# Performance work log

Hardware: AMD Instinct MI355X
Metric: run time of the kernel (lower is better)

The kernel has to match this reference:

```python
import jax, jax.numpy as jnp
import numpy as np
from jax.ops import segment_sum, segment_max

N_NODES = 50000
N_GRAPHS = 64
EPS = 1e-16


def gat_layer(x, src, dst, W, a_src, a_dst, b, n_nodes):
    # PyG GATConv, heads=1: shared linear, additive attention, per-dst softmax
    h = x @ W                                  # [N, H]
    al_s = h @ a_src                           # [N]
    al_d = h @ a_dst                           # [N]
    e = jax.nn.leaky_relu(al_s[src] + al_d[dst], 0.2)   # [E]
    # numerically stable segment softmax over edges grouped by dst
    m = segment_max(e, dst, num_segments=n_nodes)
    m = jnp.where(jnp.isfinite(m), m, 0.0)
    ex = jnp.exp(e - m[dst])
    denom = segment_sum(ex, dst, num_segments=n_nodes)
    alpha = ex / (denom[dst] + EPS)            # [E]
    out = segment_sum(alpha[:, None] * h[src], dst, num_segments=n_nodes)
    return out + b


def setup_inputs() -> dict:
    key = jax.random.key(0)
    ks = jax.random.split(key, 16)
    H = 128
    x = jax.random.normal(ks[0], (N_NODES, 4), dtype=jnp.float32)
    edge_index = jax.random.randint(ks[1], (2, 800000), 0, N_NODES, dtype=jnp.int64)
    batch = jnp.sort(jax.random.randint(ks[2], (N_NODES,), 0, N_GRAPHS, dtype=jnp.int64))

    def glorot(k, shape):
        lim = np.sqrt(6.0 / (shape[0] + shape[-1]))
        return jax.random.uniform(k, shape, jnp.float32, -lim, lim)

    params = {
        'W1': glorot(ks[3], (4, H)), 'as1': glorot(ks[4], (H,)), 'ad1': glorot(ks[5], (H,)), 'b1': jnp.zeros((H,), jnp.float32),
        'W2': glorot(ks[6], (H, H)), 'as2': glorot(ks[7], (H,)), 'ad2': glorot(ks[8], (H,)), 'b2': jnp.zeros((H,), jnp.float32),
        'W3': glorot(ks[9], (H, H)), 'as3': glorot(ks[10], (H,)), 'ad3': glorot(ks[11], (H,)), 'b3': jnp.zeros((H,), jnp.float32),
        'Wlin': glorot(ks[12], (H, 2)), 'blin': jnp.zeros((2,), jnp.float32),
    }
    return {'x': x, 'edge_index': edge_index, 'batch': batch, **params}


def reference(x, edge_index, batch, W1, as1, ad1, b1, W2, as2, ad2, b2, W3, as3, ad3, b3, Wlin, blin):
    n = x.shape[0]
    # GATConv default add_self_loops=True
    loop = jnp.arange(n, dtype=edge_index.dtype)
    src = jnp.concatenate([edge_index[0], loop])
    dst = jnp.concatenate([edge_index[1], loop])

    h = jax.nn.relu(gat_layer(x, src, dst, W1, as1, ad1, b1, n))
    h = jax.nn.relu(gat_layer(h, src, dst, W2, as2, ad2, b2, n))
    h = gat_layer(h, src, dst, W3, as3, ad3, b3, n)

    # global_mean_pool
    sums = segment_sum(h, batch, num_segments=N_GRAPHS)          # [G, H]
    cnt = segment_sum(jnp.ones((n,), h.dtype), batch, num_segments=N_GRAPHS)
    pooled = sums / jnp.maximum(cnt, 1.0)[:, None]
    # dropout p=0.5 is identity in eval mode
    return pooled @ Wlin + blin                                   # [G, 2]
```

## Files before the change

kernel.cpp:

```cpp
#include <hip/hip_runtime.h>
#include <math.h>


#define BW 512
#define PART_CHUNK 4096
#define HIST_WGS 64

typedef __attribute__((ext_vector_type(8))) short short8v;
typedef __attribute__((ext_vector_type(4))) float f32x4;
typedef __attribute__((ext_vector_type(4))) unsigned uint4v;
typedef __attribute__((ext_vector_type(2))) unsigned uint2v;

__device__ int g_hist_ctr;

__device__ __forceinline__ float bflo(unsigned u) { return __uint_as_float(u << 16); }
__device__ __forceinline__ float bfhi(unsigned u) { return __uint_as_float(u & 0xffff0000u); }
__device__ __forceinline__ unsigned pk2bf(float a, float b) {
  unsigned ua = __float_as_uint(a); ua += 0x7fffu + ((ua >> 16) & 1u);
  unsigned ub = __float_as_uint(b); ub += 0x7fffu + ((ub >> 16) & 1u);
  return (ua >> 16) | (ub & 0xffff0000u);
}

__global__ __launch_bounds__(256) void kb_hist(const int* __restrict__ ei,
                                               int* __restrict__ bpart,
                                               int* __restrict__ bbase,
                                               int* __restrict__ bcur,
                                               int* __restrict__ rowp,
                                               int E, int ET, int N, int NB) {
  __shared__ int h[128];
  __shared__ int isLast;
  int tid = threadIdx.x;
  if (tid < 128) h[tid] = 0;
  __syncthreads();
  int stride = HIST_WGS * 256;
  for (int i = blockIdx.x * 256 + tid; i < ET; i += stride) {
    int dst = (i < E) ? ei[E + i] : (i - E);
    atomicAdd(&h[dst >> 9], 1);
  }
  __syncthreads();
  if (tid < 128) bpart[blockIdx.x * 128 + tid] = h[tid];
  __threadfence();
  if (tid == 0) {
    int old = atomicAdd(&g_hist_ctr, 1);
    isLast = (((old + 1) % HIST_WGS) == 0) ? 1 : 0;
  }
  __syncthreads();
  if (isLast) {
    __shared__ int sm[128];
    int v = 0;
    if (tid < 128) {
      for (int w = 0; w < HIST_WGS; ++w)
        v += atomicAdd(&bpart[w * 128 + tid], 0);
      if (tid >= NB) v = 0;
      sm[tid] = v;
    }
    __syncthreads();
    for (int off = 1; off < 128; off <<= 1) {
      int u = (tid < 128 && tid >= off) ? sm[tid - off] : 0;
      __syncthreads();
      if (tid < 128) sm[tid] += u;
      __syncthreads();
    }
    if (tid < 128) {
      int pre = sm[tid] - v;
      if (tid <= NB) bbase[tid] = pre;
      if (tid < NB) bcur[tid] = pre;
      if (tid == 0) rowp[N] = ET;
    }
  }
}

__global__ __launch_bounds__(256) void kb_part(const int* __restrict__ ei,
                                               int* __restrict__ bcur,
                                               int* __restrict__ bucketed,
                                               int E, int ET, int NB) {
  __shared__ int hist[128];
  __shared__ int runb[128];
  int tid = threadIdx.x;
  int base = blockIdx.x * PART_CHUNK;
  if (tid < 128) hist[tid] = 0;

  int sv[16], dv[16];
#pragma unroll
  for (int k = 0; k < 16; ++k) {
    int j = base + k * 256 + tid;
    int s = -1, d = 0;
    if (j < ET) {
      if (j < E) { s = ei[j]; d = ei[E + j]; }
      else       { s = j - E; d = j - E; }
    }
    sv[k] = s; dv[k] = d;
  }
  __syncthreads();
#pragma unroll
  for (int k = 0; k < 16; ++k)
    if (sv[k] >= 0) atomicAdd(&hist[dv[k] >> 9], 1);
  __syncthreads();
  if (tid < NB && hist[tid] > 0) runb[tid] = atomicAdd(&bcur[tid], hist[tid]);
  __syncthreads();
  if (tid < 128) hist[tid] = 0;
  __syncthreads();
#pragma unroll
  for (int k = 0; k < 16; ++k) {
    if (sv[k] >= 0) {
      int b = dv[k] >> 9;
      int off = atomicAdd(&hist[b], 1);
      bucketed[runb[b] + off] = (sv[k] << 9) | (dv[k] & (BW - 1));
    }
  }
}

__global__ __launch_bounds__(256) void kb_csrprep(const int* __restrict__ bucketed,
                                                  const int* __restrict__ bbase,
                                                  int* __restrict__ rowp,
                                                  int* __restrict__ csr,
                                                  const float* __restrict__ W2,
                                                  const float* __restrict__ W3,
                                                  const float* __restrict__ W1,
                                                  const float* __restrict__ as1,
                                                  const float* __restrict__ ad1,
                                                  unsigned short* __restrict__ Wcm2,
                                                  unsigned short* __restrict__ Wcm3,
                                                  float* __restrict__ wv,
                                                  float* __restrict__ gsum,
                                                  int N, int NB) {
  int tid = threadIdx.x;
  if ((int)blockIdx.x >= NB) {
    int pb = blockIdx.x - NB;
    if (pb >= 65) {
      int idx = (pb - 65) * 256 + tid;
      if (idx < 64 * 128 + 64) gsum[idx] = 0.f;
      return;
    }
    if (pb == 64) {
      if (tid >= 64) return;
      float2 a = *(const float2*)(as1 + tid * 2);
      float2 d = *(const float2*)(ad1 + tid * 2);
      float ps[4], pd[4];
#pragma unroll
      for (int k = 0; k < 4; ++k) {
        float2 w = *(const float2*)(W1 + k * 128 + tid * 2);
        ps[k] = w.x * a.x + w.y * a.y;
        pd[k] = w.x * d.x + w.y * d.y;
      }
      for (int off = 32; off; off >>= 1) {
#pragma unroll
        for (int k = 0; k < 4; ++k) {
          ps[k] += __shfl_xor(ps[k], off);
          pd[k] += __shfl_xor(pd[k], off);
        }
      }
      if (tid == 0) {
#pragma unroll
        for (int k = 0; k < 4; ++k) { wv[k] = ps[k]; wv[4 + k] = pd[k]; }
      }
      return;
    }
    int i = pb * 256 + tid;
    if (i < 16384) {
      int k = i >> 7, n = i & 127;
      unsigned u = __float_as_uint(W2[i]); u += 0x7fffu + ((u >> 16) & 1u);
      Wcm2[n * 128 + k] = (unsigned short)(u >> 16);
      unsigned v = __float_as_uint(W3[i]); v += 0x7fffu + ((v >> 16) & 1u);
      Wcm3[n * 128 + k] = (unsigned short)(v >> 16);
    }
    return;
  }
  __shared__ int h[512];
  __shared__ int sm[256];
  __shared__ int cur[512];
  int b = blockIdx.x;
  int cb = bbase[b], ce = bbase[b + 1];

  h[tid] = 0; h[tid + 256] = 0;
  __syncthreads();
  for (int j = cb + tid; j < ce; j += 256)
    atomicAdd(&h[bucketed[j] & (BW - 1)], 1);
  __syncthreads();
  int a0 = h[2 * tid], a1 = h[2 * tid + 1];
  int s = a0 + a1;
  sm[tid] = s;
  __syncthreads();
  for (int off = 1; off < 256; off <<= 1) {
    int u = (tid >= off) ? sm[tid - off] : 0;
    __syncthreads();
    sm[tid] += u;
    __syncthreads();
  }
  int pre = sm[tid] - s;
  cur[2 * tid] = pre;
  cur[2 * tid + 1] = pre + a0;
  __syncthreads();
  int node0 = b * BW;
  for (int local = tid; local < BW; local += 256) {
    int node = node0 + local;
    if (node < N) rowp[node] = cb + cur[local];
  }
  __syncthreads();
  for (int j = cb + tid; j < ce; j += 256) {
    int p = bucketed[j];
    int loc = p & (BW - 1);
    int pos = cb + atomicAdd(&cur[loc], 1);
    csr[pos] = (unsigned)p >> 9;
  }
}

__device__ __forceinline__ void agg_full64(int beg, int end, float ald, int dst,
    const int* __restrict__ csr_src, const float* __restrict__ al_s,
    const uint4* __restrict__ Hbf, const float* __restrict__ bias,
    float* __restrict__ exw, unsigned* __restrict__ Ybf, int relu) {
  int lane = threadIdx.x & 63;
  int deg = end - beg;
  int q = lane >> 4, l = lane & 15;
  float acc[8];
#pragma unroll
  for (int c = 0; c < 8; ++c) acc[c] = 0.f;

  if (deg <= 64) {
    int srcv = 0;
    float e = -INFINITY;
    if (lane < deg) {
      srcv = csr_src[beg + lane];
      e = al_s[srcv] + ald;
      e = (e > 0.f) ? e : 0.2f * e;
    }
    float m = e;
    for (int off = 32; off; off >>= 1) m = fmaxf(m, __shfl_xor(m, off));
    float av = (lane < deg) ? __expf(e - m) : 0.f;
    float den = av;
    for (int off = 32; off; off >>= 1) den += __shfl_xor(den, off);
    av *= 1.0f / (den + 1e-16f);
    for (int t = 0; t < deg; t += 4) {
      int sA = __shfl(srcv, t + q);
      float wA = __shfl(av, t + q);
      uint4 va = Hbf[(size_t)sA * 16 + l];
      acc[0] += wA * bflo(va.x); acc[1] += wA * bfhi(va.x);
      acc[2] += wA * bflo(va.y); acc[3] += wA * bfhi(va.y);
      acc[4] += wA * bflo(va.z); acc[5] += wA * bfhi(va.z);
      acc[6] += wA * bflo(va.w); acc[7] += wA * bfhi(va.w);
    }
  } else {
    float m = -INFINITY;
    for (int j = beg + lane; j < end; j += 64) {
      float e = al_s[csr_src[j]] + ald;
      e = (e > 0.f) ? e : 0.2f * e;
      exw[j] = e;
      m = fmaxf(m, e);
    }
    for (int off = 32; off; off >>= 1) m = fmaxf(m, __shfl_xor(m, off));
    float den = 0.f;
    for (int j = beg + lane; j < end; j += 64) {
      float ex = __expf(exw[j] - m);
      exw[j] = ex;
      den += ex;
    }
    for (int off = 32; off; off >>= 1) den += __shfl_xor(den, off);
    float inv = 1.0f / (den + 1e-16f);
    for (int j = beg + q; j < end; j += 4) {
      int sA = csr_src[j];
      float wA = exw[j] * inv;
      uint4 va = Hbf[(size_t)sA * 16 + l];
      acc[0] += wA * bflo(va.x); acc[1] += wA * bfhi(va.x);
      acc[2] += wA * bflo(va.y); acc[3] += wA * bfhi(va.y);
      acc[4] += wA * bflo(va.z); acc[5] += wA * bfhi(va.z);
      acc[6] += wA * bflo(va.w); acc[7] += wA * bfhi(va.w);
    }
  }
#pragma unroll
  for (int c = 0; c < 8; ++c) {
    acc[c] += __shfl_xor(acc[c], 16);
    acc[c] += __shfl_xor(acc[c], 32);
  }
  if (q == 0) {
    float4 bv0 = *(const float4*)(bias + l * 8);
    float4 bv1 = *(const float4*)(bias + l * 8 + 4);
    float o0 = acc[0] + bv0.x, o1 = acc[1] + bv0.y, o2 = acc[2] + bv0.z, o3 = acc[3] + bv0.w;
    float o4 = acc[4] + bv1.x, o5 = acc[5] + bv1.y, o6 = acc[6] + bv1.z, o7 = acc[7] + bv1.w;
    if (relu) {
      o0 = fmaxf(o0, 0.f); o1 = fmaxf(o1, 0.f); o2 = fmaxf(o2, 0.f); o3 = fmaxf(o3, 0.f);
      o4 = fmaxf(o4, 0.f); o5 = fmaxf(o5, 0.f); o6 = fmaxf(o6, 0.f); o7 = fmaxf(o7, 0.f);
    }
    uint4v pb;
    pb.x = pk2bf(o0, o1); pb.y = pk2bf(o2, o3);
    pb.z = pk2bf(o4, o5); pb.w = pk2bf(o6, o7);
    __builtin_nontemporal_store(pb, (uint4v*)(Ybf + (size_t)dst * 64 + l * 4));
  }
}

__device__ __forceinline__ void aggx1_full64(int beg, int end, float ald, int dst,
    const int* __restrict__ csr_src, const float* __restrict__ X,
    float wvs0, float wvs1, float wvs2, float wvs3,
    const float* __restrict__ W, const float* __restrict__ bias,
    float* __restrict__ exw, unsigned* __restrict__ Ybf) {
  int lane = threadIdx.x & 63;
  int deg = end - beg;
  float4 acc = {0.f, 0.f, 0.f, 0.f};
  if (deg <= 64) {
    int srcv = 0;
    float e = -INFINITY;
    float4 xv = {0.f, 0.f, 0.f, 0.f};
    if (lane < deg) {
      srcv = csr_src[beg + lane];
      xv = *(const float4*)(X + (size_t)srcv * 4);
      e = xv.x * wvs0 + xv.y * wvs1 + xv.z * wvs2 + xv.w * wvs3 + ald;
      e = (e > 0.f) ? e : 0.2f * e;
    }
    float m = e;
    for (int off = 32; off; off >>= 1) m = fmaxf(m, __shfl_xor(m, off));
    float av = (lane < deg) ? __expf(e - m) : 0.f;
    float den = av;
    for (int off = 32; off; off >>= 1) den += __shfl_xor(den, off);
    av *= 1.0f / (den + 1e-16f);
    acc.x = av * xv.x; acc.y = av * xv.y; acc.z = av * xv.z; acc.w = av * xv.w;
  } else {
    float m = -INFINITY;
    for (int j = beg + lane; j < end; j += 64) {
      int s = csr_src[j];
      float4 xv = *(const float4*)(X + (size_t)s * 4);
      float e = xv.x * wvs0 + xv.y * wvs1 + xv.z * wvs2 + xv.w * wvs3 + ald;
      e = (e > 0.f) ? e : 0.2f * e;
      exw[j] = e;
      m = fmaxf(m, e);
    }
    for (int off = 32; off; off >>= 1) m = fmaxf(m, __shfl_xor(m, off));
    float den = 0.f;
    for (int j = beg + lane; j < end; j += 64) {
      float ex = __expf(exw[j] - m);
      exw[j] = ex;
      den += ex;
    }
    for (int off = 32; off; off >>= 1) den += __shfl_xor(den, off);
    float inv = 1.0f / (den + 1e-16f);
    for (int j = beg + lane; j < end; j += 64) {
      int s = csr_src[j];
      float w = exw[j] * inv;
      float4 xv = *(const float4*)(X + (size_t)s * 4);
      acc.x += w * xv.x; acc.y += w * xv.y; acc.z += w * xv.z; acc.w += w * xv.w;
    }
  }
  for (int off = 32; off; off >>= 1) {
    acc.x += __shfl_xor(acc.x, off);
    acc.y += __shfl_xor(acc.y, off);
    acc.z += __shfl_xor(acc.z, off);
    acc.w += __shfl_xor(acc.w, off);
  }
  int f = lane * 2;
  float2 w0 = *(const float2*)(W + f);
  float2 w1 = *(const float2*)(W + 128 + f);
  float2 w2 = *(const float2*)(W + 256 + f);
  float2 w3 = *(const float2*)(W + 384 + f);
  float2 bv = *(const float2*)(bias + f);
  float h0 = acc.x * w0.x + acc.y * w1.x + acc.z * w2.x + acc.w * w3.x + bv.x;
  float h1 = acc.x * w0.y + acc.y * w1.y + acc.z * w2.y + acc.w * w3.y + bv.y;
  h0 = fmaxf(h0, 0.f); h1 = fmaxf(h1, 0.f);
  __builtin_nontemporal_store(pk2bf(h0, h1), Ybf + (size_t)dst * 64 + lane);
}

__global__ __launch_bounds__(256) void k_aggx1(const int* __restrict__ csr_src,
                                               const int* __restrict__ rowp,
                                               const float* __restrict__ wv,
                                               const float* __restrict__ X,
                                               const float* __restrict__ W,
                                               const float* __restrict__ bias,
                                               float* __restrict__ exw,
                                               unsigned* __restrict__ Ybf, int N) {
  int wid = threadIdx.x >> 6, lane = threadIdx.x & 63;
  int half = lane >> 5, il = lane & 31;
  int d0 = blockIdx.x * 8 + wid * 2;
  if (d0 >= N) return;
  float wvs0 = wv[0], wvs1 = wv[1], wvs2 = wv[2], wvs3 = wv[3];
  float wvd0 = wv[4], wvd1 = wv[5], wvd2 = wv[6], wvd3 = wv[7];

  int dst = d0 + half;
  bool vdst = dst < N;
  int beg = 0, end = 0;
  if (vdst) { beg = rowp[dst]; end = rowp[dst + 1]; }
  int deg = end - beg;
  int mx = max(deg, __shfl_xor(deg, 32));

  float ald = 0.f;
  if (vdst) {
    float4 xd = *(const float4*)(X + (size_t)dst * 4);
    ald = xd.x * wvd0 + xd.y * wvd1 + xd.z * wvd2 + xd.w * wvd3;
  }

  if (mx <= 32) {
    int srcv = 0;
    float e = -INFINITY;
    float4 xv = {0.f, 0.f, 0.f, 0.f};
    if (il < deg) {
      srcv = csr_src[beg + il];
      xv = *(const float4*)(X + (size_t)srcv * 4);
      float e0 = xv.x * wvs0 + xv.y * wvs1 + xv.z * wvs2 + xv.w * wvs3 + ald;
      e = (e0 > 0.f) ? e0 : 0.2f * e0;
    }
    float m = e;
    for (int off = 16; off; off >>= 1) m = fmaxf(m, __shfl_xor(m, off));
    float av = (il < deg) ? __expf(e - m) : 0.f;
    float den = av;
    for (int off = 16; off; off >>= 1) den += __shfl_xor(den, off);
    av *= 1.0f / (den + 1e-16f);
    float4 acc;
    acc.x = av * xv.x; acc.y = av * xv.y; acc.z = av * xv.z; acc.w = av * xv.w;
    for (int off = 16; off; off >>= 1) {
      acc.x += __shfl_xor(acc.x, off);
      acc.y += __shfl_xor(acc.y, off);
      acc.z += __shfl_xor(acc.z, off);
      acc.w += __shfl_xor(acc.w, off);
    }
    int f = il * 4;
    float4 w0 = *(const float4*)(W + f);
    float4 w1 = *(const float4*)(W + 128 + f);
    float4 w2 = *(const float4*)(W + 256 + f);
    float4 w3 = *(const float4*)(W + 384 + f);
    float4 bv = *(const float4*)(bias + f);
    float h0 = acc.x * w0.x + acc.y * w1.x + acc.z * w2.x + acc.w * w3.x + bv.x;
    float h1 = acc.x * w0.y + acc.y * w1.y + acc.z * w2.y + acc.w * w3.y + bv.y;
    float h2 = acc.x * w0.z + acc.y * w1.z + acc.z * w2.z + acc.w * w3.z + bv.z;
    float h3 = acc.x * w0.w + acc.y * w1.w + acc.z * w2.w + acc.w * w3.w + bv.w;
    h0 = fmaxf(h0, 0.f); h1 = fmaxf(h1, 0.f);
    h2 = fmaxf(h2, 0.f); h3 = fmaxf(h3, 0.f);
    if (vdst) {
      uint2v pb;
      pb.x = pk2bf(h0, h1); pb.y = pk2bf(h2, h3);
      __builtin_nontemporal_store(pb, (uint2v*)(Ybf + (size_t)dst * 64 + il * 2));
    }
  } else {
    for (int k = 0; k < 2; ++k) {
      int d = d0 + k;
      if (d < N) {
        int b = rowp[d], en = rowp[d + 1];
        float4 xd = *(const float4*)(X + (size_t)d * 4);
        float a2 = xd.x * wvd0 + xd.y * wvd1 + xd.z * wvd2 + xd.w * wvd3;
        aggx1_full64(b, en, a2, d, csr_src, X, wvs0, wvs1, wvs2, wvs3, W, bias, exw, Ybf);
      }
    }
  }
}

__global__ __launch_bounds__(256) void k_gemm128mfma(
    const unsigned short* __restrict__ Xbf,
    const unsigned short* __restrict__ Wcm,
    const float* __restrict__ asv, const float* __restrict__ adv,
    unsigned* __restrict__ Hbf,
    float* __restrict__ al_s, float* __restrict__ al_d, int N) {
  int wid = threadIdx.x >> 6, lane = threadIdx.x & 63;
  int c = lane & 15, g = lane >> 4;
  int row0 = blockIdx.x * 64 + wid * 16;
  int arow = row0 + c;
  int arowc = (arow < N) ? arow : (N - 1);

  short8v a[4];
#pragma unroll
  for (int kt = 0; kt < 4; ++kt)
    a[kt] = *(const short8v*)(Xbf + (size_t)arowc * 128 + kt * 32 + g * 8);

  f32x4 acc[8];
#pragma unroll
  for (int f = 0; f < 8; ++f) acc[f] = (f32x4){0.f, 0.f, 0.f, 0.f};

#pragma unroll
  for (int f = 0; f < 8; ++f) {
    const unsigned short* wb = Wcm + (size_t)(f * 16 + c) * 128 + g * 8;
#pragma unroll
    for (int kt = 0; kt < 4; ++kt) {
      short8v b = *(const short8v*)(wb + kt * 32);
      acc[f] = __builtin_amdgcn_mfma_f32_16x16x32_bf16(a[kt], b, acc[f], 0, 0, 0);
    }
  }

  float ps[4] = {0.f, 0.f, 0.f, 0.f}, pd[4] = {0.f, 0.f, 0.f, 0.f};
#pragma unroll
  for (int f = 0; f < 8; ++f) {
    float as_c = asv[f * 16 + c], ad_c = adv[f * 16 + c];
#pragma unroll
    for (int j = 0; j < 4; ++j) { ps[j] += acc[f][j] * as_c; pd[j] += acc[f][j] * ad_c; }
  }
#pragma unroll
  for (int j = 0; j < 4; ++j) {
    for (int off = 1; off < 16; off <<= 1) {
      ps[j] += __shfl_xor(ps[j], off);
      pd[j] += __shfl_xor(pd[j], off);
    }
  }
  if (c == 0) {
#pragma unroll
    for (int j = 0; j < 4; ++j) {
      int r = row0 + g * 4 + j;
      if (r < N) { al_s[r] = ps[j]; al_d[r] = pd[j]; }
    }
  }

#pragma unroll
  for (int f = 0; f < 8; ++f) {
#pragma unroll
    for (int j = 0; j < 4; ++j) {
      float partner = __shfl_xor(acc[f][j], 1);
      int r = row0 + g * 4 + j;
      if (((lane & 1) == 0) && r < N)
        __builtin_nontemporal_store(pk2bf(acc[f][j], partner),
                                    Hbf + (size_t)r * 64 + f * 8 + (c >> 1));
    }
  }
}

__global__ __launch_bounds__(256) void k_agg(const int* __restrict__ csr_src,
                                             const int* __restrict__ rowp,
                                             const float* __restrict__ al_s,
                                             const float* __restrict__ al_d,
                                             const uint4* __restrict__ Hbf,
                                             const float* __restrict__ bias,
                                             float* __restrict__ exw,
                                             unsigned* __restrict__ Ybf,
                                             int N, int relu) {
  int wid = threadIdx.x >> 6, lane = threadIdx.x & 63;
  int half = lane >> 5, il = lane & 31;
  int d0 = blockIdx.x * 8 + wid * 2;
  if (d0 >= N) return;
  int dst = d0 + half;
  bool vdst = dst < N;
  int beg = 0, end = 0;
  if (vdst) { beg = rowp[dst]; end = rowp[dst + 1]; }
  int deg = end - beg;
  int mx = max(deg, __shfl_xor(deg, 32));
  float ald = vdst ? al_d[dst] : 0.f;

  if (mx <= 32) {
    int srcv = 0;
    float e = -INFINITY;
    if (il < deg) {
      srcv = csr_src[beg + il];
      e = al_s[srcv] + ald;
      e = (e > 0.f) ? e : 0.2f * e;
    }
    float m = e;
    for (int off = 16; off; off >>= 1) m = fmaxf(m, __shfl_xor(m, off));
    float av = (il < deg) ? __expf(e - m) : 0.f;
    float den = av;
    for (int off = 16; off; off >>= 1) den += __shfl_xor(den, off);
    av *= 1.0f / (den + 1e-16f);

    int q = il >> 4, l = il & 15;
    int b32 = lane & 32;
    float acc[8];
#pragma unroll
    for (int c = 0; c < 8; ++c) acc[c] = 0.f;

#pragma unroll
    for (int gbase = 0; gbase < 32; gbase += 16) {
      int s[8]; float w[8];
#pragma unroll
      for (int k = 0; k < 8; ++k) {
        int slot = b32 + gbase + k * 2 + q;
        s[k] = __shfl(srcv, slot);
        w[k] = __shfl(av, slot);
      }
      uint4 v[8];
#pragma unroll
      for (int k = 0; k < 8; ++k) v[k] = Hbf[(size_t)s[k] * 16 + l];
#pragma unroll
      for (int k = 0; k < 8; ++k) {
        acc[0] += w[k] * bflo(v[k].x); acc[1] += w[k] * bfhi(v[k].x);
        acc[2] += w[k] * bflo(v[k].y); acc[3] += w[k] * bfhi(v[k].y);
        acc[4] += w[k] * bflo(v[k].z); acc[5] += w[k] * bfhi(v[k].z);
        acc[6] += w[k] * bflo(v[k].w); acc[7] += w[k] * bfhi(v[k].w);
      }
    }
#pragma unroll
    for (int c = 0; c < 8; ++c) acc[c] += __shfl_xor(acc[c], 16);
    if (q == 0 && vdst) {
      float4 bv0 = *(const float4*)(bias + l * 8);
      float4 bv1 = *(const float4*)(bias + l * 8 + 4);
      float o0 = acc[0] + bv0.x, o1 = acc[1] + bv0.y, o2 = acc[2] + bv0.z, o3 = acc[3] + bv0.w;
      float o4 = acc[4] + bv1.x, o5 = acc[5] + bv1.y, o6 = acc[6] + bv1.z, o7 = acc[7] + bv1.w;
      if (relu) {
        o0 = fmaxf(o0, 0.f); o1 = fmaxf(o1, 0.f); o2 = fmaxf(o2, 0.f); o3 = fmaxf(o3, 0.f);
        o4 = fmaxf(o4, 0.f); o5 = fmaxf(o5, 0.f); o6 = fmaxf(o6, 0.f); o7 = fmaxf(o7, 0.f);
      }
      uint4v pb;
      pb.x = pk2bf(o0, o1); pb.y = pk2bf(o2, o3);
      pb.z = pk2bf(o4, o5); pb.w = pk2bf(o6, o7);
      __builtin_nontemporal_store(pb, (uint4v*)(Ybf + (size_t)dst * 64 + l * 4));
    }
  } else {
    for (int k = 0; k < 2; ++k) {
      int d = d0 + k;
      if (d < N) {
        int b = rowp[d], en = rowp[d + 1];
        agg_full64(b, en, al_d[d], d, csr_src, al_s, Hbf, bias, exw, Ybf, relu);
      }
    }
  }
}

__global__ __launch_bounds__(256) void k_pool(const unsigned* __restrict__ Ybf,
                                              const int* __restrict__ batch,
                                              float* __restrict__ gsum,
                                              float* __restrict__ gcnt,
                                              int N, int nwaves) {
  int gw = (blockIdx.x * 256 + threadIdx.x) >> 6;
  int lane = threadIdx.x & 63;
  int chunk = (N + nwaves - 1) / nwaves;
  int beg = gw * chunk;
  int end = beg + chunk; if (end > N) end = N;
  if (beg >= end) return;

  int curg = batch[beg];
  float2 acc = {0.f, 0.f};
  int cnt = 0;
  for (int n = beg; n < end; ++n) {
    int g = batch[n];
    if (g != curg) {
      atomicAdd(&gsum[curg * 128 + lane * 2], acc.x);
      atomicAdd(&gsum[curg * 128 + lane * 2 + 1], acc.y);
      if (lane == 0) atomicAdd(&gcnt[curg], (float)cnt);
      acc.x = 0.f; acc.y = 0.f; cnt = 0; curg = g;
    }
    unsigned u = Ybf[(size_t)n * 64 + lane];
    acc.x += bflo(u); acc.y += bfhi(u);
    ++cnt;
  }
  atomicAdd(&gsum[curg * 128 + lane * 2], acc.x);
  atomicAdd(&gsum[curg * 128 + lane * 2 + 1], acc.y);
  if (lane == 0) atomicAdd(&gcnt[curg], (float)cnt);
}

__global__ __launch_bounds__(128) void k_final(const float* __restrict__ gsum,
                                               const float* __restrict__ gcnt,
                                               const float* __restrict__ Wlin,
                                               const float* __restrict__ blin,
                                               float* __restrict__ out) {
  int t = threadIdx.x;
  int g = t >> 1, c = t & 1;
  float inv = 1.0f / fmaxf(gcnt[g], 1.0f);
  float acc = blin[c];
  for (int k = 0; k < 128; ++k) acc += gsum[g * 128 + k] * inv * Wlin[k * 2 + c];
  out[g * 2 + c] = acc;
}

extern "C" void kernel_launch(void* const* d_in, const int* in_sizes, int n_in,
                              void* d_out, int out_size, void* d_ws, size_t ws_size,
                              hipStream_t stream) {
  const float* x    = (const float*)d_in[0];
  const int*   ei   = (const int*)d_in[1];
  const int*   batch= (const int*)d_in[2];
  const float* W1   = (const float*)d_in[3];
  const float* as1  = (const float*)d_in[4];
  const float* ad1  = (const float*)d_in[5];
  const float* b1   = (const float*)d_in[6];
  const float* W2   = (const float*)d_in[7];
  const float* as2  = (const float*)d_in[8];
  const float* ad2  = (const float*)d_in[9];
  const float* b2   = (const float*)d_in[10];
  const float* W3   = (const float*)d_in[11];
  const float* as3  = (const float*)d_in[12];
  const float* ad3  = (const float*)d_in[13];
  const float* b3   = (const float*)d_in[14];
  const float* Wlin = (const float*)d_in[15];
  const float* blin = (const float*)d_in[16];

  int N = in_sizes[0] / 4;
  int E = in_sizes[1] / 2;
  int ET = E + N;
  int NB = (N + BW - 1) / BW;

  char* ws = (char*)d_ws;
  unsigned* bfA = (unsigned*)ws; ws += (size_t)N * 64 * 4;
  unsigned* bfB = (unsigned*)ws; ws += (size_t)N * 64 * 4;
  float* al_s = (float*)ws; ws += (size_t)N * 4;
  float* al_d = (float*)ws; ws += (size_t)N * 4;
  float* wv   = (float*)ws; ws += (size_t)64 * 4;
  float* gsum = (float*)ws; ws += (size_t)64 * 128 * 4;
  float* gcnt = (float*)ws; ws += (size_t)64 * 4;
  int* rowp   = (int*)ws;   ws += (size_t)(N + 1) * 4;
  int* csr    = (int*)ws;   ws += (size_t)ET * 4;
  float* exw  = (float*)ws; ws += (size_t)ET * 4;
  int* bucketed = (int*)ws; ws += (size_t)ET * 4;
  int* bpart  = (int*)ws;   ws += (size_t)HIST_WGS * 128 * 4;
  int* bbase  = (int*)ws;   ws += (size_t)132 * 4;
  int* bcur   = (int*)ws;   ws += (size_t)128 * 4;
  unsigned short* wcm2 = (unsigned short*)ws; ws += (size_t)128 * 128 * 2;
  unsigned short* wcm3 = (unsigned short*)ws; ws += (size_t)128 * 128 * 2;

  kb_hist<<<HIST_WGS, 256, 0, stream>>>(ei, bpart, bbase, bcur, rowp, E, ET, N, NB);
  kb_part<<<(ET + PART_CHUNK - 1) / PART_CHUNK, 256, 0, stream>>>(ei, bcur, bucketed, E, ET, NB);
  kb_csrprep<<<NB + 98, 256, 0, stream>>>(bucketed, bbase, rowp, csr,
                                          W2, W3, W1, as1, ad1, wcm2, wcm3, wv, gsum, N, NB);

  int nb8 = (N + 7) / 8;
  int nb64 = (N + 63) / 64;
  k_aggx1<<<nb8, 256, 0, stream>>>(csr, rowp, wv, x, W1, b1, exw, bfB, N);
  k_gemm128mfma<<<nb64, 256, 0, stream>>>((const unsigned short*)bfB, wcm2, as2, ad2, bfA, al_s, al_d, N);
  k_agg        <<<nb8, 256, 0, stream>>>(csr, rowp, al_s, al_d, (const uint4*)bfA, b2, exw, bfB, N, 1);
  k_gemm128mfma<<<nb64, 256, 0, stream>>>((const unsigned short*)bfB, wcm3, as3, ad3, bfA, al_s, al_d, N);
  k_agg        <<<nb8, 256, 0, stream>>>(csr, rowp, al_s, al_d, (const uint4*)bfA, b3, exw, bfB, N, 0);

  k_pool <<<256, 256, 0, stream>>>(bfB, batch, gsum, gcnt, N, 1024);
  k_final<<<1, 128, 0, stream>>>(gsum, gcnt, Wlin, blin, (float*)d_out);
}
```

Before: 309.4 us.

## Split aggregation into alpha softmax kernel and feature-sliced gather kernel

The fused softmax-plus-aggregate kernel for layers 2 and 3 is replaced by two kernels. The first computes per-edge normalized attention weights into a buffer. The second launches 8 blocks per destination group, each gathering a 16-feature slice of source rows, with 16 edges handled in parallel per half-wave. The goal is more parallelism and better cache locality for the feature-dim gather. The cost is an extra launch, an extra pass over the alpha array, and csr/alpha being re-read once per slice.

```diff
diff --git a/kernel.cpp b/kernel.cpp
--- a/kernel.cpp
+++ b/kernel.cpp
@@ -205,88 +205,6 @@
   }
 }
 
-__device__ __forceinline__ void agg_full64(int beg, int end, float ald, int dst,
-    const int* __restrict__ csr_src, const float* __restrict__ al_s,
-    const uint4* __restrict__ Hbf, const float* __restrict__ bias,
-    float* __restrict__ exw, unsigned* __restrict__ Ybf, int relu) {
-  int lane = threadIdx.x & 63;
-  int deg = end - beg;
-  int q = lane >> 4, l = lane & 15;
-  float acc[8];
-#pragma unroll
-  for (int c = 0; c < 8; ++c) acc[c] = 0.f;
-
-  if (deg <= 64) {
-    int srcv = 0;
-    float e = -INFINITY;
-    if (lane < deg) {
-      srcv = csr_src[beg + lane];
-      e = al_s[srcv] + ald;
-      e = (e > 0.f) ? e : 0.2f * e;
-    }
-    float m = e;
-    for (int off = 32; off; off >>= 1) m = fmaxf(m, __shfl_xor(m, off));
-    float av = (lane < deg) ? __expf(e - m) : 0.f;
-    float den = av;
-    for (int off = 32; off; off >>= 1) den += __shfl_xor(den, off);
-    av *= 1.0f / (den + 1e-16f);
-    for (int t = 0; t < deg; t += 4) {
-      int sA = __shfl(srcv, t + q);
-      float wA = __shfl(av, t + q);
-      uint4 va = Hbf[(size_t)sA * 16 + l];
-      acc[0] += wA * bflo(va.x); acc[1] += wA * bfhi(va.x);
-      acc[2] += wA * bflo(va.y); acc[3] += wA * bfhi(va.y);
-      acc[4] += wA * bflo(va.z); acc[5] += wA * bfhi(va.z);
-      acc[6] += wA * bflo(va.w); acc[7] += wA * bfhi(va.w);
-    }
-  } else {
-    float m = -INFINITY;
-    for (int j = beg + lane; j < end; j += 64) {
-      float e = al_s[csr_src[j]] + ald;
-      e = (e > 0.f) ? e : 0.2f * e;
-      exw[j] = e;
-      m = fmaxf(m, e);
-    }
-    for (int off = 32; off; off >>= 1) m = fmaxf(m, __shfl_xor(m, off));
-    float den = 0.f;
-    for (int j = beg + lane; j < end; j += 64) {
-      float ex = __expf(exw[j] - m);
-      exw[j] = ex;
-      den += ex;
-    }
-    for (int off = 32; off; off >>= 1) den += __shfl_xor(den, off);
-    float inv = 1.0f / (den + 1e-16f);
-    for (int j = beg + q; j < end; j += 4) {
-      int sA = csr_src[j];
-      float wA = exw[j] * inv;
-      uint4 va = Hbf[(size_t)sA * 16 + l];
-      acc[0] += wA * bflo(va.x); acc[1] += wA * bfhi(va.x);
-      acc[2] += wA * bflo(va.y); acc[3] += wA * bfhi(va.y);
-      acc[4] += wA * bflo(va.z); acc[5] += wA * bfhi(va.z);
-      acc[6] += wA * bflo(va.w); acc[7] += wA * bfhi(va.w);
-    }
-  }
-#pragma unroll
-  for (int c = 0; c < 8; ++c) {
-    acc[c] += __shfl_xor(acc[c], 16);
-    acc[c] += __shfl_xor(acc[c], 32);
-  }
-  if (q == 0) {
-    float4 bv0 = *(const float4*)(bias + l * 8);
-    float4 bv1 = *(const float4*)(bias + l * 8 + 4);
-    float o0 = acc[0] + bv0.x, o1 = acc[1] + bv0.y, o2 = acc[2] + bv0.z, o3 = acc[3] + bv0.w;
-    float o4 = acc[4] + bv1.x, o5 = acc[5] + bv1.y, o6 = acc[6] + bv1.z, o7 = acc[7] + bv1.w;
-    if (relu) {
-      o0 = fmaxf(o0, 0.f); o1 = fmaxf(o1, 0.f); o2 = fmaxf(o2, 0.f); o3 = fmaxf(o3, 0.f);
-      o4 = fmaxf(o4, 0.f); o5 = fmaxf(o5, 0.f); o6 = fmaxf(o6, 0.f); o7 = fmaxf(o7, 0.f);
-    }
-    uint4v pb;
-    pb.x = pk2bf(o0, o1); pb.y = pk2bf(o2, o3);
-    pb.z = pk2bf(o4, o5); pb.w = pk2bf(o6, o7);
-    __builtin_nontemporal_store(pb, (uint4v*)(Ybf + (size_t)dst * 64 + l * 4));
-  }
-}
-
 __device__ __forceinline__ void aggx1_full64(int beg, int end, float ald, int dst,
     const int* __restrict__ csr_src, const float* __restrict__ X,
     float wvs0, float wvs1, float wvs2, float wvs3,
@@ -504,15 +422,11 @@
   }
 }
 
-__global__ __launch_bounds__(256) void k_agg(const int* __restrict__ csr_src,
-                                             const int* __restrict__ rowp,
-                                             const float* __restrict__ al_s,
-                                             const float* __restrict__ al_d,
-                                             const uint4* __restrict__ Hbf,
-                                             const float* __restrict__ bias,
-                                             float* __restrict__ exw,
-                                             unsigned* __restrict__ Ybf,
-                                             int N, int relu) {
+__global__ __launch_bounds__(256) void k_alpha(const int* __restrict__ csr_src,
+                                               const int* __restrict__ rowp,
+                                               const float* __restrict__ al_s,
+                                               const float* __restrict__ al_d,
+                                               float* __restrict__ alpha, int N) {
   int wid = threadIdx.x >> 6, lane = threadIdx.x & 63;
   int half = lane >> 5, il = lane & 31;
   int d0 = blockIdx.x * 8 + wid * 2;
@@ -523,15 +437,14 @@
   if (vdst) { beg = rowp[dst]; end = rowp[dst + 1]; }
   int deg = end - beg;
   int mx = max(deg, __shfl_xor(deg, 32));
-  float ald = vdst ? al_d[dst] : 0.f;
 
   if (mx <= 32) {
-    int srcv = 0;
+    float ald = vdst ? al_d[dst] : 0.f;
     float e = -INFINITY;
+    int j = beg + il;
     if (il < deg) {
-      srcv = csr_src[beg + il];
-      e = al_s[srcv] + ald;
-      e = (e > 0.f) ? e : 0.2f * e;
+      float e0 = al_s[csr_src[j]] + ald;
+      e = (e0 > 0.f) ? e0 : 0.2f * e0;
     }
     float m = e;
     for (int off = 16; off; off >>= 1) m = fmaxf(m, __shfl_xor(m, off));
@@ -539,57 +452,105 @@
     float den = av;
     for (int off = 16; off; off >>= 1) den += __shfl_xor(den, off);
     av *= 1.0f / (den + 1e-16f);
-
-    int q = il >> 4, l = il & 15;
-    int b32 = lane & 32;
-    float acc[8];
-#pragma unroll
-    for (int c = 0; c < 8; ++c) acc[c] = 0.f;
-
-#pragma unroll
-    for (int gbase = 0; gbase < 32; gbase += 16) {
-      int s[8]; float w[8];
-#pragma unroll
-      for (int k = 0; k < 8; ++k) {
-        int slot = b32 + gbase + k * 2 + q;
-        s[k] = __shfl(srcv, slot);
-        w[k] = __shfl(av, slot);
-      }
-      uint4 v[8];
-#pragma unroll
-      for (int k = 0; k < 8; ++k) v[k] = Hbf[(size_t)s[k] * 16 + l];
-#pragma unroll
-      for (int k = 0; k < 8; ++k) {
-        acc[0] += w[k] * bflo(v[k].x); acc[1] += w[k] * bfhi(v[k].x);
-        acc[2] += w[k] * bflo(v[k].y); acc[3] += w[k] * bfhi(v[k].y);
-        acc[4] += w[k] * bflo(v[k].z); acc[5] += w[k] * bfhi(v[k].z);
-        acc[6] += w[k] * bflo(v[k].w); acc[7] += w[k] * bfhi(v[k].w);
-      }
-    }
-#pragma unroll
-    for (int c = 0; c < 8; ++c) acc[c] += __shfl_xor(acc[c], 16);
-    if (q == 0 && vdst) {
-      float4 bv0 = *(const float4*)(bias + l * 8);
-      float4 bv1 = *(const float4*)(bias + l * 8 + 4);
-      float o0 = acc[0] + bv0.x, o1 = acc[1] + bv0.y, o2 = acc[2] + bv0.z, o3 = acc[3] + bv0.w;
-      float o4 = acc[4] + bv1.x, o5 = acc[5] + bv1.y, o6 = acc[6] + bv1.z, o7 = acc[7] + bv1.w;
-      if (relu) {
-        o0 = fmaxf(o0, 0.f); o1 = fmaxf(o1, 0.f); o2 = fmaxf(o2, 0.f); o3 = fmaxf(o3, 0.f);
-        o4 = fmaxf(o4, 0.f); o5 = fmaxf(o5, 0.f); o6 = fmaxf(o6, 0.f); o7 = fmaxf(o7, 0.f);
-      }
-      uint4v pb;
-      pb.x = pk2bf(o0, o1); pb.y = pk2bf(o2, o3);
-      pb.z = pk2bf(o4, o5); pb.w = pk2bf(o6, o7);
-      __builtin_nontemporal_store(pb, (uint4v*)(Ybf + (size_t)dst * 64 + l * 4));
-    }
+    if (il < deg) alpha[j] = av;
   } else {
     for (int k = 0; k < 2; ++k) {
       int d = d0 + k;
-      if (d < N) {
-        int b = rowp[d], en = rowp[d + 1];
-        agg_full64(b, en, al_d[d], d, csr_src, al_s, Hbf, bias, exw, Ybf, relu);
+      if (d >= N) continue;
+      int b = rowp[d], en = rowp[d + 1];
+      int dg = en - b;
+      float a2 = al_d[d];
+      if (dg <= 64) {
+        float e = -INFINITY;
+        int j = b + lane;
+        if (lane < dg) {
+          float e0 = al_s[csr_src[j]] + a2;
+          e = (e0 > 0.f) ? e0 : 0.2f * e0;
+        }
+        float m = e;
+        for (int off = 32; off; off >>= 1) m = fmaxf(m, __shfl_xor(m, off));
+        float av = (lane < dg) ? __expf(e - m) : 0.f;
+        float den = av;
+        for (int off = 32; off; off >>= 1) den += __shfl_xor(den, off);
+        av *= 1.0f / (den + 1e-16f);
+        if (lane < dg) alpha[j] = av;
+      } else {
+        float m = -INFINITY;
+        for (int j = b + lane; j < en; j += 64) {
+          float e = al_s[csr_src[j]] + a2;
+          e = (e > 0.f) ? e : 0.2f * e;
+          alpha[j] = e;
+          m = fmaxf(m, e);
+        }
+        for (int off = 32; off; off >>= 1) m = fmaxf(m, __shfl_xor(m, off));
+        float den = 0.f;
+        for (int j = b + lane; j < en; j += 64) {
+          float ex = __expf(alpha[j] - m);
+          alpha[j] = ex;
+          den += ex;
+        }
+        for (int off = 32; off; off >>= 1) den += __shfl_xor(den, off);
+        float inv = 1.0f / (den + 1e-16f);
+        for (int j = b + lane; j < en; j += 64) alpha[j] *= inv;
       }
     }
+  }
+}
+
+__global__ __launch_bounds__(256) void k_aggs(const int* __restrict__ csr_src,
+                                              const int* __restrict__ rowp,
+                                              const float* __restrict__ alpha,
+                                              const uint4* __restrict__ Hbf,
+                                              const float* __restrict__ bias,
+                                              unsigned* __restrict__ Ybf,
+                                              int N, int relu) {
+  int slice = blockIdx.x & 7;
+  int dgroup = blockIdx.x >> 3;
+  int wid = threadIdx.x >> 6, lane = threadIdx.x & 63;
+  int half = lane >> 5, il = lane & 31;
+  int dst = dgroup * 8 + wid * 2 + half;
+  if (dst >= N) return;
+  int beg = rowp[dst], end = rowp[dst + 1];
+  int deg = end - beg;
+  int es = il >> 1, b = il & 1;
+  const uint4* Hcol = Hbf + slice * 2 + b;
+
+  float acc[8];
+#pragma unroll
+  for (int c = 0; c < 8; ++c) acc[c] = 0.f;
+
+  for (int t = 0; t < deg; t += 16) {
+    int edge = t + es;
+    bool v = edge < deg;
+    int s = 0; float w = 0.f;
+    if (v) { s = csr_src[beg + edge]; w = alpha[beg + edge]; }
+    uint4 vv = Hcol[(size_t)s * 16];
+    acc[0] += w * bflo(vv.x); acc[1] += w * bfhi(vv.x);
+    acc[2] += w * bflo(vv.y); acc[3] += w * bfhi(vv.y);
+    acc[4] += w * bflo(vv.z); acc[5] += w * bfhi(vv.z);
+    acc[6] += w * bflo(vv.w); acc[7] += w * bfhi(vv.w);
+  }
+#pragma unroll
+  for (int c = 0; c < 8; ++c) {
+    acc[c] += __shfl_xor(acc[c], 2);
+    acc[c] += __shfl_xor(acc[c], 4);
+    acc[c] += __shfl_xor(acc[c], 8);
+    acc[c] += __shfl_xor(acc[c], 16);
+  }
+  if (es == 0) {
+    int f = slice * 16 + b * 8;
+    float4 bv0 = *(const float4*)(bias + f);
+    float4 bv1 = *(const float4*)(bias + f + 4);
+    float o0 = acc[0] + bv0.x, o1 = acc[1] + bv0.y, o2 = acc[2] + bv0.z, o3 = acc[3] + bv0.w;
+    float o4 = acc[4] + bv1.x, o5 = acc[5] + bv1.y, o6 = acc[6] + bv1.z, o7 = acc[7] + bv1.w;
+    if (relu) {
+      o0 = fmaxf(o0, 0.f); o1 = fmaxf(o1, 0.f); o2 = fmaxf(o2, 0.f); o3 = fmaxf(o3, 0.f);
+      o4 = fmaxf(o4, 0.f); o5 = fmaxf(o5, 0.f); o6 = fmaxf(o6, 0.f); o7 = fmaxf(o7, 0.f);
+    }
+    uint4v pb;
+    pb.x = pk2bf(o0, o1); pb.y = pk2bf(o2, o3);
+    pb.z = pk2bf(o4, o5); pb.w = pk2bf(o6, o7);
+    __builtin_nontemporal_store(pb, (uint4v*)(Ybf + (size_t)dst * 64 + (slice * 2 + b) * 4));
   }
 }
 
@@ -691,9 +652,11 @@
   int nb64 = (N + 63) / 64;
   k_aggx1<<<nb8, 256, 0, stream>>>(csr, rowp, wv, x, W1, b1, exw, bfB, N);
   k_gemm128mfma<<<nb64, 256, 0, stream>>>((const unsigned short*)bfB, wcm2, as2, ad2, bfA, al_s, al_d, N);
-  k_agg        <<<nb8, 256, 0, stream>>>(csr, rowp, al_s, al_d, (const uint4*)bfA, b2, exw, bfB, N, 1);
+  k_alpha<<<nb8, 256, 0, stream>>>(csr, rowp, al_s, al_d, exw, N);
+  k_aggs <<<nb8 * 8, 256, 0, stream>>>(csr, rowp, exw, (const uint4*)bfA, b2, bfB, N, 1);
   k_gemm128mfma<<<nb64, 256, 0, stream>>>((const unsigned short*)bfB, wcm3, as3, ad3, bfA, al_s, al_d, N);
-  k_agg        <<<nb8, 256, 0, stream>>>(csr, rowp, al_s, al_d, (const uint4*)bfA, b3, exw, bfB, N, 0);
+  k_alpha<<<nb8, 256, 0, stream>>>(csr, rowp, al_s, al_d, exw, N);
+  k_aggs <<<nb8 * 8, 256, 0, stream>>>(csr, rowp, exw, (const uint4*)bfA, b3, bfB, N, 0);
 
   k_pool <<<256, 256, 0, stream>>>(bfB, batch, gsum, gcnt, N, 1024);
   k_final<<<1, 128, 0, stream>>>(gsum, gcnt, Wlin, blin, (float*)d_out);
```

Result: slower. 437.6 us (+41.4%).
